# Kernel optimization log

Hardware: AMD Instinct MI355X
Metric: run time of the kernel (lower is better)

## Reference

```python
import jax, jax.numpy as jnp
import numpy as np

B, T, V, E, H, FC, O = 4096, 64, 512, 32, 128, 256, 1024


def setup_inputs() -> dict:
    key = jax.random.key(0)
    ks = jax.random.split(key, 12)
    n = lambda k, shape, sc=1.0: (jax.random.normal(k, shape, jnp.float32) * sc)
    return {
        "message": n(ks[0], (B, T, V), 0.1),
        "W_emb": n(ks[1], (E, V), 0.05),
        "b_emb": n(ks[2], (E,), 0.05),
        "init_emb": n(ks[3], (1, 1, E), 1.0),
        "W_ih": n(ks[4], (3 * H, E), 0.08),
        "W_hh": n(ks[5], (3 * H, H), 0.08),
        "b_ih": n(ks[6], (3 * H,), 0.05),
        "b_hh": n(ks[7], (3 * H,), 0.05),
        "W_fc1": n(ks[8], (FC, H), 0.08),
        "b_fc1": n(ks[9], (FC,), 0.05),
        "W_fc2": n(ks[10], (O, FC), 0.05),
        "b_fc2": n(ks[11], (O,), 0.05),
    }


def reference(message, W_emb, b_emb, init_emb, W_ih, W_hh, b_ih, b_hh,
              W_fc1, b_fc1, W_fc2, b_fc2):
    Bb, Tt, Vv = message.shape
    Hh = W_hh.shape[1]
    # Per-step embedding of the message (torch does this inside the loop;
    # it is a pure per-timestep linear so we batch it once): [B,T,E]
    emb = jnp.einsum('btv,ev->bte', message, W_emb) + b_emb
    # Inputs consumed by the GRU at step t: initial_embedding at t=0,
    # then embedding(message[:, t-1]) for t >= 1. The embedding of the
    # final token is computed in torch but never fed to the GRU.
    x0 = jnp.broadcast_to(init_emb[0], (Bb, init_emb.shape[-1]))  # [B,E]
    xs = jnp.concatenate([x0[:, None, :], emb[:, :Tt - 1, :]], axis=1)  # [B,T,E]
    # Precompute input-side gate pre-activations for all steps: [T,B,3H]
    gi_all = jnp.einsum('bte,ge->tbg', xs, W_ih) + b_ih

    def gru_step(h, gi):
        gh = h @ W_hh.T + b_hh  # [B,3H]
        i_r, i_z, i_n = jnp.split(gi, 3, axis=-1)
        h_r, h_z, h_n = jnp.split(gh, 3, axis=-1)
        r = jax.nn.sigmoid(i_r + h_r)
        z = jax.nn.sigmoid(i_z + h_z)
        nng = jnp.tanh(i_n + r * h_n)
        h_new = (1.0 - z) * nng + z * h
        return h_new, None

    h0 = jnp.zeros((Bb, Hh), message.dtype)
    h_last, _ = jax.lax.scan(gru_step, h0, gi_all)
    hid = jax.nn.elu(h_last @ W_fc1.T + b_fc1)
    return jax.nn.sigmoid(hid @ W_fc2.T + b_fc2)
```

## Files before the change

### kernel.cpp

```cpp
#include <hip/hip_runtime.h>
#include <math.h>

#define B_ 4096
#define T_ 64
#define V_ 512
#define E_ 32
#define H_ 128
#define FC1_ 256
#define O_ 1024

typedef float f32x4 __attribute__((ext_vector_type(4)));
typedef short s16x8 __attribute__((ext_vector_type(8)));
typedef unsigned short u16;

#define MFMA16(a, b, c) __builtin_amdgcn_mfma_f32_16x16x32_bf16(a, b, c, 0, 0, 0)

#define LDS_BARRIER() do {                                   \
    asm volatile("s_waitcnt lgkmcnt(0)" ::: "memory");       \
    __builtin_amdgcn_s_barrier();                            \
} while (0)

union Frag { u16 q[8]; s16x8 v; };

__device__ __forceinline__ u16 f2bf(float f) {
    union { float f; unsigned u; } v; v.f = f;
    unsigned r = v.u + 0x7FFFu + ((v.u >> 16) & 1u);
    return (u16)(r >> 16);
}
__device__ __forceinline__ float sigf(float x) { return 1.0f / (1.0f + __expf(-x)); }
__device__ __forceinline__ float tanhfast(float x) {
    return 1.0f - 2.0f / (__expf(2.0f * x) + 1.0f);
}

__global__ void __launch_bounds__(256) prep_kernel(
    const float* __restrict__ Wih, const float* __restrict__ Whh,
    const float* __restrict__ Wemb, const float* __restrict__ Wfc1,
    const float* __restrict__ Wfc2,
    u16* __restrict__ wihF, u16* __restrict__ whhF, u16* __restrict__ wembF,
    u16* __restrict__ wfc1F, u16* __restrict__ wfc2F) {
    int id = blockIdx.x * 256 + threadIdx.x;
    int np = gridDim.x * 256;
    for (int i = id; i < 24 * 4 * 64 * 8; i += np) {
        int j = i & 7, l = (i >> 3) & 63, kc = (i >> 9) & 3, gt = i >> 11;
        whhF[i] = f2bf(Whh[(gt * 16 + (l & 15)) * 128 + kc * 32 + (l >> 4) * 8 + j]);
    }
    for (int i = id; i < 24 * 64 * 8; i += np) {
        int j = i & 7, l = (i >> 3) & 63, gt = i >> 9;
        wihF[i] = f2bf(Wih[(gt * 16 + (l & 15)) * 32 + (l >> 4) * 8 + j]);
    }
    for (int i = id; i < 2 * 16 * 64 * 8; i += np) {
        int j = i & 7, l = (i >> 3) & 63, kc = (i >> 9) & 15, nt = i >> 13;
        wembF[i] = f2bf(Wemb[(nt * 16 + (l & 15)) * 512 + kc * 32 + (l >> 4) * 8 + j]);
    }
    for (int i = id; i < 16 * 4 * 64 * 8; i += np) {
        int j = i & 7, l = (i >> 3) & 63, kc = (i >> 9) & 3, ot = i >> 11;
        wfc1F[i] = f2bf(Wfc1[(ot * 16 + (l & 15)) * 128 + kc * 32 + (l >> 4) * 8 + j]);
    }
    for (int i = id; i < 64 * 8 * 64 * 8; i += np) {
        int j = i & 7, l = (i >> 3) & 63, kc = (i >> 9) & 7, nt = i >> 12;
        wfc2F[i] = f2bf(Wfc2[(nt * 16 + (l & 15)) * 256 + kc * 32 + (l >> 4) * 8 + j]);
    }
}

__global__ void __launch_bounds__(512, 2) fused_kernel(
    const float* __restrict__ msg,
    const u16* __restrict__ whhF8, const u16* __restrict__ wihF8,
    const u16* __restrict__ wembF8,
    const float* __restrict__ b_ih, const float* __restrict__ b_hh,
    const float* __restrict__ b_emb, const float* __restrict__ init_emb,
    const u16* __restrict__ wfc1F8, const float* __restrict__ b_fc1,
    const u16* __restrict__ wfc2F8, const float* __restrict__ b_fc2,
    float* __restrict__ out) {
    __shared__ u16 hlds[2][16 * 136];
    __shared__ float epart[8][16 * 36];
    __shared__ u16 xfrag[16 * 40];
    __shared__ u16 hidl[16 * 264];
    const int tid = threadIdx.x, w = tid >> 6, l = tid & 63;
    const int ln = l & 15, lh = l >> 4;
    const int wg = w & 3, wp = w >> 2;
    const int gb = blockIdx.x;

    for (int i = tid; i < 16 * 136; i += 512) hlds[0][i] = 0;

    const s16x8* whhFv = (const s16x8*)whhF8;
    const s16x8* wihFv = (const s16x8*)wihF8;
    const s16x8* wembFv = (const s16x8*)wembF8;
    s16x8 wh[3][4], wi[3], we[2][2];
    float br, bz, bin, bgn;
    {
        #pragma unroll
        for (int g = 0; g < 3; g++) {
            int gt = wg + 4 * wp + 8 * g;
            #pragma unroll
            for (int kc = 0; kc < 4; kc++) wh[g][kc] = whhFv[(gt * 4 + kc) * 64 + l];
            wi[g] = wihFv[gt * 64 + l];
        }
        int c = wg * 16 + wp * 64 + ln;
        br  = b_ih[c] + b_hh[c];
        bz  = b_ih[128 + c] + b_hh[128 + c];
        bin = b_ih[256 + c];
        bgn = b_hh[256 + c];
        #pragma unroll
        for (int kk = 0; kk < 2; kk++) {
            we[kk][0] = wembFv[(2 * w + kk) * 64 + l];
            we[kk][1] = wembFv[(16 + 2 * w + kk) * 64 + l];
        }
    }
    const float bev = b_emb[tid & 31];

    s16x8 xcur;
    {
        Frag xi;
        #pragma unroll
        for (int j = 0; j < 8; j++) xi.q[j] = f2bf(init_emb[lh * 8 + j]);
        xcur = xi.v;
    }
    float hold[4] = {};
    const float* mrow = msg + (size_t)(gb * 16 + ln) * T_ * V_ + (2 * w) * 32 + lh * 8;
    f32x4 mb0[4], mb1[4], mb2[4], mb3[4];
#define LOADCOL(BUF, C) do {                                   \
    const float* p_ = mrow + (size_t)(C) * 512;                \
    BUF[0] = *(const f32x4*)(p_);                              \
    BUF[1] = *(const f32x4*)(p_ + 4);                          \
    BUF[2] = *(const f32x4*)(p_ + 32);                         \
    BUF[3] = *(const f32x4*)(p_ + 36);                         \
} while (0)
    LOADCOL(mb0, 0); LOADCOL(mb1, 1); LOADCOL(mb2, 2);
    LDS_BARRIER();

    const int aoff = ln * 136 + lh * 8;
    const int colo = wg * 16 + wp * 64 + ln;

#define GRU_STEP(T, MC, MN) do {                                               \
    const int t = (T);                                                         \
    if (t <= 59) LOADCOL(MN, t + 3);                                           \
    const u16* hb = hlds[t & 1];                                               \
    s16x8 af0 = *(const s16x8*)(hb + aoff);                                    \
    s16x8 af1 = *(const s16x8*)(hb + aoff + 32);                               \
    s16x8 af2 = *(const s16x8*)(hb + aoff + 64);                               \
    s16x8 af3 = *(const s16x8*)(hb + aoff + 96);                               \
    f32x4 ar  = {br, br, br, br};                                              \
    f32x4 az  = {bz, bz, bz, bz};                                              \
    f32x4 agn = {bgn, bgn, bgn, bgn};                                          \
    f32x4 ain = {bin, bin, bin, bin};                                          \
    ar  = MFMA16(xcur, wi[0], ar);                                             \
    az  = MFMA16(xcur, wi[1], az);                                             \
    ain = MFMA16(xcur, wi[2], ain);                                            \
    ar  = MFMA16(af0, wh[0][0], ar);                                           \
    ar  = MFMA16(af1, wh[0][1], ar);                                           \
    ar  = MFMA16(af2, wh[0][2], ar);                                           \
    ar  = MFMA16(af3, wh[0][3], ar);                                           \
    az  = MFMA16(af0, wh[1][0], az);                                           \
    az  = MFMA16(af1, wh[1][1], az);                                           \
    az  = MFMA16(af2, wh[1][2], az);                                           \
    az  = MFMA16(af3, wh[1][3], az);                                           \
    agn = MFMA16(af0, wh[2][0], agn);                                          \
    agn = MFMA16(af1, wh[2][1], agn);                                          \
    agn = MFMA16(af2, wh[2][2], agn);                                          \
    agn = MFMA16(af3, wh[2][3], agn);                                          \
    u16* hw = hlds[(t + 1) & 1];                                               \
    _Pragma("unroll")                                                          \
    for (int i = 0; i < 4; i++) {                                              \
        float rg = sigf(ar[i]);                                                \
        float zg = sigf(az[i]);                                                \
        float ng = tanhfast(ain[i] + rg * agn[i]);                             \
        float hn = zg * (hold[i] - ng) + ng;                                   \
        hold[i] = hn;                                                          \
        hw[(lh * 4 + i) * 136 + colo] = f2bf(hn);                              \
    }                                                                          \
    if (t < 63) {                                                              \
        f32x4 e0 = {0.f, 0.f, 0.f, 0.f}, e1 = {0.f, 0.f, 0.f, 0.f};            \
        _Pragma("unroll")                                                      \
        for (int kk = 0; kk < 2; kk++) {                                       \
            Frag fa;                                                           \
            _Pragma("unroll")                                                  \
            for (int j = 0; j < 4; j++) {                                      \
                fa.q[j]     = f2bf(MC[2 * kk][j]);                             \
                fa.q[4 + j] = f2bf(MC[2 * kk + 1][j]);                         \
            }                                                                  \
            e0 = MFMA16(fa.v, we[kk][0], e0);                                  \
            e1 = MFMA16(fa.v, we[kk][1], e1);                                  \
        }                                                                      \
        _Pragma("unroll")                                                      \
        for (int i = 0; i < 4; i++) {                                          \
            epart[w][(lh * 4 + i) * 36 + ln]      = e0[i];                     \
            epart[w][(lh * 4 + i) * 36 + 16 + ln] = e1[i];                     \
        }                                                                      \
    }                                                                          \
    LDS_BARRIER();                                                             \
    if (t < 63) {                                                              \
        int fr = tid >> 5, fc = tid & 31, fo = fr * 36 + fc;                   \
        float s = epart[0][fo] + epart[1][fo] + epart[2][fo] + epart[3][fo]    \
                + epart[4][fo] + epart[5][fo] + epart[6][fo] + epart[7][fo]    \
                + bev;                                                         \
        xfrag[fr * 40 + fc] = f2bf(s);                                         \
        LDS_BARRIER();                                                         \
        xcur = *(const s16x8*)(xfrag + ln * 40 + lh * 8);                      \
    }                                                                          \
} while (0)

    for (int tt = 0; tt < 64; tt += 4) {
        GRU_STEP(tt + 0, mb0, mb3);
        GRU_STEP(tt + 1, mb1, mb0);
        GRU_STEP(tt + 2, mb2, mb1);
        GRU_STEP(tt + 3, mb3, mb2);
    }
#undef GRU_STEP
#undef LOADCOL

    const u16* hb = hlds[0];
    s16x8 hf0 = *(const s16x8*)(hb + aoff);
    s16x8 hf1 = *(const s16x8*)(hb + aoff + 32);
    s16x8 hf2 = *(const s16x8*)(hb + aoff + 64);
    s16x8 hf3 = *(const s16x8*)(hb + aoff + 96);
    const s16x8* w1v = (const s16x8*)wfc1F8;
    #pragma unroll
    for (int q = 0; q < 2; q++) {
        int ot = 2 * w + q;
        float b1 = b_fc1[ot * 16 + ln];
        f32x4 a1 = {b1, b1, b1, b1};
        a1 = MFMA16(hf0, w1v[(ot * 4 + 0) * 64 + l], a1);
        a1 = MFMA16(hf1, w1v[(ot * 4 + 1) * 64 + l], a1);
        a1 = MFMA16(hf2, w1v[(ot * 4 + 2) * 64 + l], a1);
        a1 = MFMA16(hf3, w1v[(ot * 4 + 3) * 64 + l], a1);
        #pragma unroll
        for (int i = 0; i < 4; i++) {
            float v = a1[i];
            v = v > 0.0f ? v : (__expf(v) - 1.0f);
            hidl[(lh * 4 + i) * 264 + ot * 16 + ln] = f2bf(v);
        }
    }
    LDS_BARRIER();

    s16x8 hf[8];
    #pragma unroll
    for (int kc = 0; kc < 8; kc++)
        hf[kc] = *(const s16x8*)(hidl + ln * 264 + kc * 32 + lh * 8);
    const s16x8* w2v = (const s16x8*)wfc2F8;
    #pragma unroll
    for (int q = 0; q < 8; q++) {
        int nt = 8 * w + q;
        float b2 = b_fc2[nt * 16 + ln];
        f32x4 a2 = {b2, b2, b2, b2};
        #pragma unroll
        for (int kc = 0; kc < 8; kc++)
            a2 = MFMA16(hf[kc], w2v[(nt * 8 + kc) * 64 + l], a2);
        #pragma unroll
        for (int i = 0; i < 4; i++)
            out[(size_t)(gb * 16 + lh * 4 + i) * 1024 + nt * 16 + ln] = sigf(a2[i]);
    }
}

extern "C" void kernel_launch(void* const* d_in, const int* in_sizes, int n_in,
                              void* d_out, int out_size, void* d_ws, size_t ws_size,
                              hipStream_t stream) {
    const float* message  = (const float*)d_in[0];
    const float* W_emb    = (const float*)d_in[1];
    const float* b_emb    = (const float*)d_in[2];
    const float* init_emb = (const float*)d_in[3];
    const float* W_ih     = (const float*)d_in[4];
    const float* W_hh     = (const float*)d_in[5];
    const float* b_ih     = (const float*)d_in[6];
    const float* b_hh     = (const float*)d_in[7];
    const float* W_fc1    = (const float*)d_in[8];
    const float* b_fc1    = (const float*)d_in[9];
    const float* W_fc2    = (const float*)d_in[10];
    const float* b_fc2    = (const float*)d_in[11];
    float* out = (float*)d_out;

    u16* whhF  = (u16*)d_ws;
    u16* wihF  = whhF  + 49152;
    u16* wembF = wihF  + 12288;
    u16* wfc1F = wembF + 16384;
    u16* wfc2F = wfc1F + 32768;

    hipLaunchKernelGGL(prep_kernel, dim3(256), dim3(256), 0, stream,
                       W_ih, W_hh, W_emb, W_fc1, W_fc2, wihF, whhF, wembF, wfc1F, wfc2F);
    hipLaunchKernelGGL(fused_kernel, dim3(256), dim3(512), 0, stream,
                       message, whhF, wihF, wembF, b_ih, b_hh, b_emb, init_emb,
                       wfc1F, b_fc1, wfc2F, b_fc2, out);
}
```

Before: 138.1 us.

## Software-pipeline embedding reduction to drop one barrier per GRU step

Double-buffers the embedding partial sums and the reduced x fragment so the cross-wave reduction for step t+1 runs in the same barrier interval as the GRU update of step t. The embedding is computed one step ahead, which removes the second LDS barrier per timestep. It also deepens the message prefetch by one column. Float-to-bf16 conversions now use the packed v_cvt_pk_bf16_f32 instruction. The cost is more LDS usage, more registers, and more complex indexing.

```diff
diff --git a/kernel.cpp b/kernel.cpp
--- a/kernel.cpp
+++ b/kernel.cpp
@@ -20,12 +20,17 @@
     __builtin_amdgcn_s_barrier();                            \
 } while (0)
 
-union Frag { u16 q[8]; s16x8 v; };
+union Frag { u16 q[8]; unsigned u[4]; s16x8 v; };
 
 __device__ __forceinline__ u16 f2bf(float f) {
     union { float f; unsigned u; } v; v.f = f;
     unsigned r = v.u + 0x7FFFu + ((v.u >> 16) & 1u);
     return (u16)(r >> 16);
+}
+__device__ __forceinline__ unsigned cvtpk(float lo, float hi) {
+    unsigned r;
+    asm("v_cvt_pk_bf16_f32 %0, %1, %2" : "=v"(r) : "v"(lo), "v"(hi));
+    return r;
 }
 __device__ __forceinline__ float sigf(float x) { return 1.0f / (1.0f + __expf(-x)); }
 __device__ __forceinline__ float tanhfast(float x) {
@@ -72,8 +77,8 @@
     const u16* __restrict__ wfc2F8, const float* __restrict__ b_fc2,
     float* __restrict__ out) {
     __shared__ u16 hlds[2][16 * 136];
-    __shared__ float epart[8][16 * 36];
-    __shared__ u16 xfrag[16 * 40];
+    __shared__ float epart[2][8][576];
+    __shared__ u16 xfrag[2][640];
     __shared__ u16 hidl[16 * 264];
     const int tid = threadIdx.x, w = tid >> 6, l = tid & 63;
     const int ln = l & 15, lh = l >> 4;
@@ -108,12 +113,12 @@
     }
     const float bev = b_emb[tid & 31];
 
-    s16x8 xcur;
+    s16x8 xinit;
     {
         Frag xi;
         #pragma unroll
         for (int j = 0; j < 8; j++) xi.q[j] = f2bf(init_emb[lh * 8 + j]);
-        xcur = xi.v;
+        xinit = xi.v;
     }
     float hold[4] = {};
     const float* mrow = msg + (size_t)(gb * 16 + ln) * T_ * V_ + (2 * w) * 32 + lh * 8;
@@ -125,27 +130,53 @@
     BUF[2] = *(const f32x4*)(p_ + 32);                         \
     BUF[3] = *(const f32x4*)(p_ + 36);                         \
 } while (0)
-    LOADCOL(mb0, 0); LOADCOL(mb1, 1); LOADCOL(mb2, 2);
+
+#define EMBED_STORE(MC, PAR) do {                               \
+    f32x4 e0 = {0.f, 0.f, 0.f, 0.f}, e1 = {0.f, 0.f, 0.f, 0.f}; \
+    _Pragma("unroll")                                           \
+    for (int kk = 0; kk < 2; kk++) {                            \
+        Frag fa;                                                \
+        fa.u[0] = cvtpk(MC[2 * kk][0], MC[2 * kk][1]);          \
+        fa.u[1] = cvtpk(MC[2 * kk][2], MC[2 * kk][3]);          \
+        fa.u[2] = cvtpk(MC[2 * kk + 1][0], MC[2 * kk + 1][1]);  \
+        fa.u[3] = cvtpk(MC[2 * kk + 1][2], MC[2 * kk + 1][3]);  \
+        e0 = MFMA16(fa.v, we[kk][0], e0);                       \
+        e1 = MFMA16(fa.v, we[kk][1], e1);                       \
+    }                                                           \
+    _Pragma("unroll")                                           \
+    for (int i = 0; i < 4; i++) {                               \
+        epart[PAR][w][(lh * 4 + i) * 36 + ln]      = e0[i];     \
+        epart[PAR][w][(lh * 4 + i) * 36 + 16 + ln] = e1[i];     \
+    }                                                           \
+} while (0)
+
+    LOADCOL(mb3, 0);
+    EMBED_STORE(mb3, 1);
+    LOADCOL(mb0, 1); LOADCOL(mb1, 2); LOADCOL(mb2, 3);
     LDS_BARRIER();
 
     const int aoff = ln * 136 + lh * 8;
     const int colo = wg * 16 + wp * 64 + ln;
-
-#define GRU_STEP(T, MC, MN) do {                                               \
-    const int t = (T);                                                         \
-    if (t <= 59) LOADCOL(MN, t + 3);                                           \
+    const int fr = tid >> 5, fc = tid & 31, fo = fr * 36 + fc;
+
+#define GRU_STEP(TT, MC, MN) do {                                              \
+    const int t = (TT);                                                        \
+    if (t <= 58) LOADCOL(MN, t + 4);                                           \
     const u16* hb = hlds[t & 1];                                               \
     s16x8 af0 = *(const s16x8*)(hb + aoff);                                    \
     s16x8 af1 = *(const s16x8*)(hb + aoff + 32);                               \
     s16x8 af2 = *(const s16x8*)(hb + aoff + 64);                               \
     s16x8 af3 = *(const s16x8*)(hb + aoff + 96);                               \
+    s16x8 xc;                                                                  \
+    if (t == 0) xc = xinit;                                                    \
+    else xc = *(const s16x8*)(&xfrag[(t + 1) & 1][0] + ln * 40 + lh * 8);      \
     f32x4 ar  = {br, br, br, br};                                              \
     f32x4 az  = {bz, bz, bz, bz};                                              \
     f32x4 agn = {bgn, bgn, bgn, bgn};                                          \
     f32x4 ain = {bin, bin, bin, bin};                                          \
-    ar  = MFMA16(xcur, wi[0], ar);                                             \
-    az  = MFMA16(xcur, wi[1], az);                                             \
-    ain = MFMA16(xcur, wi[2], ain);                                            \
+    ar  = MFMA16(xc, wi[0], ar);                                               \
+    az  = MFMA16(xc, wi[1], az);                                               \
+    ain = MFMA16(xc, wi[2], ain);                                              \
     ar  = MFMA16(af0, wh[0][0], ar);                                           \
     ar  = MFMA16(af1, wh[0][1], ar);                                           \
     ar  = MFMA16(af2, wh[0][2], ar);                                           \
@@ -159,44 +190,32 @@
     agn = MFMA16(af2, wh[2][2], agn);                                          \
     agn = MFMA16(af3, wh[2][3], agn);                                          \
     u16* hw = hlds[(t + 1) & 1];                                               \
+    float hn[4];                                                               \
     _Pragma("unroll")                                                          \
     for (int i = 0; i < 4; i++) {                                              \
         float rg = sigf(ar[i]);                                                \
         float zg = sigf(az[i]);                                                \
         float ng = tanhfast(ain[i] + rg * agn[i]);                             \
-        float hn = zg * (hold[i] - ng) + ng;                                   \
-        hold[i] = hn;                                                          \
-        hw[(lh * 4 + i) * 136 + colo] = f2bf(hn);                              \
+        hn[i] = zg * (hold[i] - ng) + ng;                                      \
+        hold[i] = hn[i];                                                       \
     }                                                                          \
-    if (t < 63) {                                                              \
-        f32x4 e0 = {0.f, 0.f, 0.f, 0.f}, e1 = {0.f, 0.f, 0.f, 0.f};            \
-        _Pragma("unroll")                                                      \
-        for (int kk = 0; kk < 2; kk++) {                                       \
-            Frag fa;                                                           \
-            _Pragma("unroll")                                                  \
-            for (int j = 0; j < 4; j++) {                                      \
-                fa.q[j]     = f2bf(MC[2 * kk][j]);                             \
-                fa.q[4 + j] = f2bf(MC[2 * kk + 1][j]);                         \
-            }                                                                  \
-            e0 = MFMA16(fa.v, we[kk][0], e0);                                  \
-            e1 = MFMA16(fa.v, we[kk][1], e1);                                  \
-        }                                                                      \
-        _Pragma("unroll")                                                      \
-        for (int i = 0; i < 4; i++) {                                          \
-            epart[w][(lh * 4 + i) * 36 + ln]      = e0[i];                     \
-            epart[w][(lh * 4 + i) * 36 + 16 + ln] = e1[i];                     \
-        }                                                                      \
+    {                                                                          \
+        unsigned u01 = cvtpk(hn[0], hn[1]);                                    \
+        unsigned u23 = cvtpk(hn[2], hn[3]);                                    \
+        hw[(lh * 4 + 0) * 136 + colo] = (u16)(u01 & 0xFFFFu);                  \
+        hw[(lh * 4 + 1) * 136 + colo] = (u16)(u01 >> 16);                      \
+        hw[(lh * 4 + 2) * 136 + colo] = (u16)(u23 & 0xFFFFu);                  \
+        hw[(lh * 4 + 3) * 136 + colo] = (u16)(u23 >> 16);                      \
+    }                                                                          \
+    if (t <= 61) EMBED_STORE(MC, t & 1);                                       \
+    if (t <= 62) {                                                             \
+        const float* eb = &epart[(t + 1) & 1][0][0];                           \
+        float s = eb[fo]            + eb[576 + fo]     + eb[2 * 576 + fo]      \
+                + eb[3 * 576 + fo]  + eb[4 * 576 + fo] + eb[5 * 576 + fo]      \
+                + eb[6 * 576 + fo]  + eb[7 * 576 + fo] + bev;                  \
+        xfrag[t & 1][fr * 40 + fc] = f2bf(s);                                  \
     }                                                                          \
     LDS_BARRIER();                                                             \
-    if (t < 63) {                                                              \
-        int fr = tid >> 5, fc = tid & 31, fo = fr * 36 + fc;                   \
-        float s = epart[0][fo] + epart[1][fo] + epart[2][fo] + epart[3][fo]    \
-                + epart[4][fo] + epart[5][fo] + epart[6][fo] + epart[7][fo]    \
-                + bev;                                                         \
-        xfrag[fr * 40 + fc] = f2bf(s);                                         \
-        LDS_BARRIER();                                                         \
-        xcur = *(const s16x8*)(xfrag + ln * 40 + lh * 8);                      \
-    }                                                                          \
 } while (0)
 
     for (int tt = 0; tt < 64; tt += 4) {
@@ -207,6 +226,7 @@
     }
 #undef GRU_STEP
 #undef LOADCOL
+#undef EMBED_STORE
 
     const u16* hb = hlds[0];
     s16x8 hf0 = *(const s16x8*)(hb + aoff);
```

Result: faster. 132.2 us (-4.3%).
